# Kernel tuning notes

Hardware: AMD Instinct MI355X
Metric: run time of the kernel (lower is better)

The kernel has to match this reference:

```python
import jax, jax.numpy as jnp
import numpy as np

B, S, H = 2, 1024, 2048
D = 256          # index_dimension = min(index.embedding_dimension, hidden_size)
R = 32           # LoRA rank
K = 4            # index_k neighbors per query token
N_DB = 100000    # rows in the external index


def setup_inputs() -> dict:
    key = jax.random.key(0)
    ks = jax.random.split(key, 7)
    return {
        "hidden_states": jax.random.normal(ks[0], (B, S, H), jnp.float32),
        "db_keys": jax.random.normal(ks[1], (N_DB, D), jnp.float32),
        "db_values": jax.random.normal(ks[2], (N_DB, D), jnp.float32),
        "wq_in": jax.random.normal(ks[3], (H, R), jnp.float32) * 0.02,
        "wq_out": jax.random.normal(ks[4], (R, D), jnp.float32) * 0.02,
        "wv_in": jax.random.normal(ks[5], (D, R), jnp.float32) * 0.02,
        "wv_out": jax.random.normal(ks[6], (R, H), jnp.float32) * 0.02,
    }


def reference(hidden_states, db_keys, db_values, wq_in, wq_out, wv_in, wv_out):
    b, s, h = hidden_states.shape
    d = wq_out.shape[1]
    # query LoRA projection: hidden -> r -> index_dim
    q = (hidden_states @ wq_in) @ wq_out            # [B, S, D]

    # external k-NN lookup (exact L2 top-k over index table), no_grad in torch
    qf = q.reshape(b * s, d)                        # [B*S, D]
    qn = jnp.sum(qf * qf, axis=-1, keepdims=True)   # [B*S, 1]
    kn = jnp.sum(db_keys * db_keys, axis=-1)        # [N_DB]
    dist = qn - 2.0 * (qf @ db_keys.T) + kn[None, :]  # [B*S, N_DB]
    _, idx = jax.lax.top_k(-dist, K)                # [B*S, K] nearest neighbors

    # gather KV and reshape to [B, S*K, D] (matches torch view calls)
    kv_key = jax.lax.stop_gradient(db_keys[idx]).reshape(b, s * K, d)
    kv_val = jax.lax.stop_gradient(db_values[idx]).reshape(b, s * K, d)

    # SDPA, is_causal=True with Lq != Lk: top-left aligned tril mask (j <= i)
    scale = 1.0 / np.sqrt(d).astype(np.float32)
    scores = jnp.einsum('bqd,bkd->bqk', q, kv_key) * scale  # [B, S, S*K]
    mask = jnp.arange(s * K)[None, :] <= jnp.arange(s)[:, None]
    scores = jnp.where(mask[None, :, :], scores, jnp.finfo(scores.dtype).min)
    attn = jax.nn.softmax(scores, axis=-1)
    out = jnp.einsum('bqk,bkd->bqd', attn, kv_val)  # [B, S, D]

    # value LoRA projection: index_dim -> r -> hidden
    return (out @ wv_in) @ wv_out                   # [B, S, H]
```

## Files before the change

### kernel.cpp

```cpp
#include <hip/hip_runtime.h>
#include <cfloat>

#define B_   2
#define S_   1024
#define H_   2048
#define D_   256
#define R_   32
#define K_   4
#define NDB_ 100000

#define TSEL 256
#define NSEL (B_ * TSEL)

#define NCHUNK     112
#define CHUNK_ROWS 896
#define TILES      7
#define NT         128
#define MT         64
#define KC         64
#define LSTR       68

#define NEG_INF  (-3.0e38f)
#define IDX_MAX  0x7fffffff

#define TQ 4

#define OFF_Q     0
#define OFF_KN    0x200000
#define OFF_PS    0x280000
#define OFF_PI    0x360000
#define OFF_KVV   0x280000
#define OFF_KVT   0x480000
#define OFF_AO    0x680000
#define OFF_IDX   0x880000
#define OFF_CAND  0x890000
#define OFF_DBK16 0xA00000

typedef unsigned short ushort_t;
typedef unsigned int   uint_t;
typedef __attribute__((ext_vector_type(8)))  __bf16 bf16x8;
typedef __attribute__((ext_vector_type(16))) float  f32x16;

__device__ __forceinline__ void ins4(float sc, int n, float s[4], int id[4]) {
  if (sc > s[3] || (sc == s[3] && n < id[3])) {
    s[3] = sc; id[3] = n;
#pragma unroll
    for (int k = 3; k > 0; --k) {
      if (s[k] > s[k - 1] || (s[k] == s[k - 1] && id[k] < id[k - 1])) {
        float ts = s[k]; s[k] = s[k - 1]; s[k - 1] = ts;
        int ti = id[k]; id[k] = id[k - 1]; id[k - 1] = ti;
      }
    }
  }
}

__device__ __forceinline__ uint_t bfpack(float a, float b) {
  uint_t ua = __float_as_uint(a), ub = __float_as_uint(b);
  ua = (ua + 0x7fffu + ((ua >> 16) & 1u)) >> 16;
  ub = (ub + 0x7fffu + ((ub >> 16) & 1u)) >> 16;
  return ua | (ub << 16);
}

__global__ __launch_bounds__(256) void k_compute_q(
    const float* __restrict__ hidden, const float* __restrict__ wq_in,
    const float* __restrict__ wq_out, float* __restrict__ q) {
  __shared__ float hrow[H_];
  __shared__ float part[8][R_];
  __shared__ float q1[R_];
  const int m = blockIdx.x;
  const int t = threadIdx.x;
  const float* hp = hidden + (size_t)m * H_;
  ((float4*)hrow)[t]       = ((const float4*)hp)[t];
  ((float4*)hrow)[t + 256] = ((const float4*)hp)[t + 256];
  __syncthreads();
  const int r = t & 31, c = t >> 5;
  float p = 0.f;
#pragma unroll 4
  for (int e = c * 256; e < c * 256 + 256; ++e)
    p = fmaf(hrow[e], wq_in[(size_t)e * R_ + r], p);
  part[c][r] = p;
  __syncthreads();
  if (t < R_) {
    float s = 0.f;
#pragma unroll
    for (int cc = 0; cc < 8; ++cc) s += part[cc][t];
    q1[t] = s;
  }
  __syncthreads();
  float acc = 0.f;
#pragma unroll
  for (int rr = 0; rr < R_; ++rr) acc = fmaf(q1[rr], wq_out[rr * D_ + t], acc);
  q[(size_t)m * D_ + t] = acc;
}

__global__ __launch_bounds__(256) void k_kn_cvtT(const float* __restrict__ dbk,
                                                 float* __restrict__ kn,
                                                 ushort_t* __restrict__ dbk16T) {
  __shared__ float sT[32 * 256];
  const int n32 = blockIdx.x;
  const int t = threadIdx.x;
  {
    const int r = t >> 3, tc = t & 7;
    const float* rp = dbk + (size_t)(n32 * 32 + r) * D_;
    float s = 0.f;
#pragma unroll
    for (int k = 0; k < 8; ++k) {
      const int sl = tc + 8 * k;
      const float4 v = ((const float4*)rp)[sl];
      *(float4*)&sT[(r * 64 + (sl ^ (r & 7))) * 4] = v;
      s += v.x * v.x + v.y * v.y + v.z * v.z + v.w * v.w;
    }
    s += __shfl_down(s, 4, 8);
    s += __shfl_down(s, 2, 8);
    s += __shfl_down(s, 1, 8);
    if (tc == 0) kn[n32 * 32 + r] = s;
  }
  __syncthreads();
  {
    const int l = t & 63, w = t >> 6;
    const int row = l & 31, hc = l >> 5;
    uint4* dst = (uint4*)dbk16T + (size_t)n32 * 1024;
#pragma unroll
    for (int kk = 0; kk < 4; ++kk) {
      const int ks = kk * 4 + w;
      const int c = 2 * ks + hc;
      const int s0 = (2 * c) ^ (row & 7), s1 = (2 * c + 1) ^ (row & 7);
      const float4 a = *(const float4*)&sT[(row * 64 + s0) * 4];
      const float4 b = *(const float4*)&sT[(row * 64 + s1) * 4];
      uint4 pk;
      pk.x = bfpack(a.x, a.y); pk.y = bfpack(a.z, a.w);
      pk.z = bfpack(b.x, b.y); pk.w = bfpack(b.z, b.w);
      dst[(size_t)ks * 64 + l] = pk;
    }
  }
}

__global__ __launch_bounds__(256) void k_kn(const float* __restrict__ dbk,
                                            float* __restrict__ kn) {
  const int w = threadIdx.x >> 6, l = threadIdx.x & 63;
  const int n = blockIdx.x * 4 + w;
  if (n >= NDB_) return;
  const float4 v = ((const float4*)(dbk + (size_t)n * D_))[l];
  float s = v.x * v.x + v.y * v.y + v.z * v.z + v.w * v.w;
#pragma unroll
  for (int off = 32; off; off >>= 1) s += __shfl_down(s, off);
  if (l == 0) kn[n] = s;
}

__global__ __launch_bounds__(256, 4) void k_knn_mfma(
    const float* __restrict__ q, const ushort_t* __restrict__ dbk16T,
    const float* __restrict__ kn, float* __restrict__ pscore,
    int* __restrict__ pidx) {
  __shared__ __align__(16) char smem[32768 + CHUNK_ROWS * 4];
  ushort_t* sA  = (ushort_t*)smem;
  float*    knL = (float*)(smem + 32768);

  const int fid = blockIdx.x;
  const int xcd = fid & 7, idx8 = fid >> 3;
  const int chunk = xcd + 8 * (idx8 % 14);
  const int qb = idx8 / 14;

  const int tid = threadIdx.x;
  const int wv = tid >> 6, ln = tid & 63;
  const int lm = ln & 31, lh = ln >> 5;
  const int row_base = chunk * CHUNK_ROWS;

  {
    const int m = tid & 63, cg = tid >> 6;
    const int sq = qb * MT + m;
    const float* qp = q + ((size_t)((sq >> 8) * S_ + (sq & 255))) * D_;
#pragma unroll
    for (int cc = 0; cc < 8; ++cc) {
      const int c = cg * 8 + cc;
      const float4 v0 = *(const float4*)(qp + c * 8);
      const float4 v1 = *(const float4*)(qp + c * 8 + 4);
      uint4 pk;
      pk.x = bfpack(v0.x, v0.y); pk.y = bfpack(v0.z, v0.w);
      pk.z = bfpack(v1.x, v1.y); pk.w = bfpack(v1.z, v1.w);
      *(uint4*)&sA[(m * 32 + (c ^ (m & 7))) * 8] = pk;
    }
  }
  for (int j = tid; j < CHUNK_ROWS; j += 256) {
    int rr = row_base + j; if (rr >= NDB_) rr = NDB_ - 1;
    knL[j] = kn[rr];
  }
  __syncthreads();

  float s40[4], s41[4]; int i40[4], i41[4];
#pragma unroll
  for (int k = 0; k < 4; ++k) {
    s40[k] = NEG_INF; i40[k] = IDX_MAX;
    s41[k] = NEG_INF; i41[k] = IDX_MAX;
  }

  const int sw = lm & 7;
  const int abase0 = lm * 32;
  const int abase1 = (32 + lm) * 32;
  const int nbase = wv * 32 + 4 * lh;

  for (int tile = 0; tile < TILES; ++tile) {
    const int row0 = row_base + tile * NT;
    if (row0 >= NDB_) break;
    const int nw = row0 + wv * 32;
    if (nw >= NDB_) continue;

    f32x16 acc0, acc1;
#pragma unroll
    for (int r = 0; r < 16; ++r) { acc0[r] = 0.f; acc1[r] = 0.f; }

    const ushort_t* gw = dbk16T + (size_t)(nw >> 5) * 8192 + (size_t)ln * 8;
#pragma unroll
    for (int ks = 0; ks < 16; ++ks) {
      const bf16x8 bb = *(const bf16x8*)(gw + ks * 512);
      const int cs = (2 * ks + lh) ^ sw;
      const bf16x8 a0 = *(const bf16x8*)&sA[(abase0 + cs) * 8];
      const bf16x8 a1 = *(const bf16x8*)&sA[(abase1 + cs) * 8];
      acc0 = __builtin_amdgcn_mfma_f32_32x32x16_bf16(bb, a0, acc0, 0, 0, 0);
      acc1 = __builtin_amdgcn_mfma_f32_32x32x16_bf16(bb, a1, acc1, 0, 0, 0);
    }

#pragma unroll
    for (int g = 0; g < 4; ++g) {
      float v0[4], v1[4]; int nn[4];
#pragma unroll
      for (int j = 0; j < 4; ++j) {
        const int r = g * 4 + j;
        const int off = (r & 3) + 8 * (r >> 2);
        const int nloc = nbase + off;
        const float knv = knL[tile * 128 + nloc];
        const int n = row0 + nloc;
        nn[j] = n;
        const float x0 = fmaf(2.f, acc0[r], -knv);
        const float x1 = fmaf(2.f, acc1[r], -knv);
        const bool ok = n < NDB_;
        v0[j] = ok ? x0 : NEG_INF;
        v1[j] = ok ? x1 : NEG_INF;
      }
      const float m0 = fmaxf(fmaxf(v0[0], v0[1]), fmaxf(v0[2], v0[3]));
      if (m0 >= s40[3]) {
#pragma unroll
        for (int j = 0; j < 4; ++j) ins4(v0[j], nn[j], s40, i40);
      }
      const float m1 = fmaxf(fmaxf(v1[0], v1[1]), fmaxf(v1[2], v1[3]));
      if (m1 >= s41[3]) {
#pragma unroll
        for (int j = 0; j < 4; ++j) ins4(v1[j], nn[j], s41, i41);
      }
    }
  }

  __syncthreads();
  float* cs = (float*)smem;
  int*   ci = (int*)(smem + 8192);
  {
    const int st = wv * 2 + lh;
#pragma unroll
    for (int k = 0; k < 4; ++k) {
      cs[(lm * 8 + st) * 4 + k]        = s40[k];
      ci[(lm * 8 + st) * 4 + k]        = i40[k];
      cs[((32 + lm) * 8 + st) * 4 + k] = s41[k];
      ci[((32 + lm) * 8 + st) * 4 + k] = i41[k];
    }
  }
  __syncthreads();
  if (tid < 64) {
    float fs[4]; int fi[4];
#pragma unroll
    for (int k = 0; k < 4; ++k) { fs[k] = NEG_INF; fi[k] = IDX_MAX; }
    for (int c = 0; c < 32; ++c)
      ins4(cs[tid * 32 + c], ci[tid * 32 + c], fs, fi);
    const int sq = qb * MT + tid;
    float* po = pscore + ((size_t)sq * NCHUNK + chunk) * 4;
    int*   io = pidx   + ((size_t)sq * NCHUNK + chunk) * 4;
#pragma unroll
    for (int k = 0; k < 4; ++k) { po[k] = fs[k]; io[k] = fi[k]; }
  }
}

__global__ __launch_bounds__(256) void k_knn_partial(
    const float* __restrict__ q, const float* __restrict__ dbk,
    const float* __restrict__ kn, float* __restrict__ pscore,
    int* __restrict__ pidx) {
  __shared__ float smem[3 * KC * LSTR];
  float* sA  = smem;
  float* sB0 = smem + KC * LSTR;
  float* sB1 = smem + 2 * KC * LSTR;
  const int tid = threadIdx.x;
  const int tx = tid & 15, ty = tid >> 4;
  const int chunk = blockIdx.x, qb = blockIdx.y;
  const int arq = tid >> 2;
  const int aqd = (tid & 3) * 4;
  const int brk = tid >> 1;
  const int bh  = tid & 1;
  const int bcol = ((brk >> 3) << 2) | (brk & 3);
  float* sBw = (brk & 4) ? sB1 : sB0;
  const int sq_a = qb * MT + arq;
  const float* qsrc = q + ((size_t)((sq_a >> 8) * S_ + (sq_a & 255))) * D_;
  float s4[4][4]; int i4[4][4];
#pragma unroll
  for (int a = 0; a < 4; ++a)
#pragma unroll
    for (int b = 0; b < 4; ++b) { s4[a][b] = NEG_INF; i4[a][b] = IDX_MAX; }
  const int row_base = chunk * CHUNK_ROWS;
  for (int tile = 0; tile < TILES; ++tile) {
    const int row0 = row_base + tile * NT;
    if (row0 >= NDB_) break;
    int krow = row0 + brk; if (krow >= NDB_) krow = NDB_ - 1;
    const float* ksrc = dbk + (size_t)krow * D_;
    float acc[4][8];
#pragma unroll
    for (int a = 0; a < 4; ++a)
#pragma unroll
      for (int b = 0; b < 8; ++b) acc[a][b] = 0.f;
    for (int kc = 0; kc < 4; ++kc) {
      __syncthreads();
#pragma unroll
      for (int p = 0; p < 4; ++p) {
        const int kkl = p * 16 + aqd;
        const float4 v = *(const float4*)(qsrc + kc * KC + kkl);
        sA[(kkl + 0) * LSTR + arq] = v.x;
        sA[(kkl + 1) * LSTR + arq] = v.y;
        sA[(kkl + 2) * LSTR + arq] = v.z;
        sA[(kkl + 3) * LSTR + arq] = v.w;
      }
#pragma unroll
      for (int p = 0; p < 8; ++p) {
        const int kkl = bh * 32 + p * 4;
        const float4 v = *(const float4*)(ksrc + kc * KC + kkl);
        sBw[(kkl + 0) * LSTR + bcol] = v.x;
        sBw[(kkl + 1) * LSTR + bcol] = v.y;
        sBw[(kkl + 2) * LSTR + bcol] = v.z;
        sBw[(kkl + 3) * LSTR + bcol] = v.w;
      }
      __syncthreads();
#pragma unroll 4
      for (int kk = 0; kk < KC; ++kk) {
        const float4 a  = *(const float4*)&sA [kk * LSTR + ty * 4];
        const float4 b0 = *(const float4*)&sB0[kk * LSTR + tx * 4];
        const float4 b1 = *(const float4*)&sB1[kk * LSTR + tx * 4];
        const float av[4] = {a.x, a.y, a.z, a.w};
        const float bv[8] = {b0.x, b0.y, b0.z, b0.w, b1.x, b1.y, b1.z, b1.w};
#pragma unroll
        for (int qi = 0; qi < 4; ++qi)
#pragma unroll
          for (int nj = 0; nj < 8; ++nj)
            acc[qi][nj] = fmaf(av[qi], bv[nj], acc[qi][nj]);
      }
    }
#pragma unroll
    for (int nj = 0; nj < 8; ++nj) {
      const int n = row0 + tx * 8 + nj;
      if (n < NDB_) {
        const float knj = kn[n];
        ins4(2.f * acc[0][nj] - knj, n, s4[0], i4[0]);
        ins4(2.f * acc[1][nj] - knj, n, s4[1], i4[1]);
        ins4(2.f * acc[2][nj] - knj, n, s4[2], i4[2]);
        ins4(2.f * acc[3][nj] - knj, n, s4[3], i4[3]);
      }
    }
  }
  __syncthreads();
  float* cs = smem;
  int*   ci = (int*)(smem + 64 * 65);
#pragma unroll
  for (int qi = 0; qi < 4; ++qi)
#pragma unroll
    for (int k = 0; k < 4; ++k) {
      cs[(ty * 4 + qi) * 65 + tx * 4 + k] = s4[qi][k];
      ci[(ty * 4 + qi) * 65 + tx * 4 + k] = i4[qi][k];
    }
  __syncthreads();
  if (tid < 64) {
    float fs[4]; int fi[4];
#pragma unroll
    for (int k = 0; k < 4; ++k) { fs[k] = NEG_INF; fi[k] = IDX_MAX; }
    for (int c = 0; c < 64; ++c)
      ins4(cs[tid * 65 + c], ci[tid * 65 + c], fs, fi);
    const int sq = qb * MT + tid;
    float* po = pscore + ((size_t)sq * NCHUNK + chunk) * 4;
    int*   io = pidx   + ((size_t)sq * NCHUNK + chunk) * 4;
#pragma unroll
    for (int k = 0; k < 4; ++k) { po[k] = fs[k]; io[k] = fi[k]; }
  }
}

template <int RANKS>
__device__ __forceinline__ void merge_top(const float* __restrict__ pscore,
                                          const int* __restrict__ pidx,
                                          int* __restrict__ outp) {
  const int sq = blockIdx.x, l = threadIdx.x;
  float s4[4]; int i4[4];
#pragma unroll
  for (int k = 0; k < 4; ++k) { s4[k] = NEG_INF; i4[k] = IDX_MAX; }
  for (int c = l; c < NCHUNK * 4; c += 64)
    ins4(pscore[(size_t)sq * NCHUNK * 4 + c], pidx[(size_t)sq * NCHUNK * 4 + c], s4, i4);
#pragma unroll
  for (int r = 0; r < RANKS; ++r) {
    float s = s4[0]; int i = i4[0];
#pragma unroll
    for (int off = 32; off; off >>= 1) {
      float so = __shfl_down(s, off); int io = __shfl_down(i, off);
      if (so > s || (so == s && io < i)) { s = so; i = io; }
    }
    const float sw = __shfl(s, 0); const int iw = __shfl(i, 0);
    if (l == 0) outp[sq * RANKS + r] = iw;
    if (s4[0] == sw && i4[0] == iw) {
      s4[0] = s4[1]; i4[0] = i4[1];
      s4[1] = s4[2]; i4[1] = i4[2];
      s4[2] = s4[3]; i4[2] = i4[3];
      s4[3] = NEG_INF; i4[3] = IDX_MAX;
    }
  }
}

__global__ __launch_bounds__(64) void k_knn_merge4(const float* __restrict__ ps,
                                                   const int* __restrict__ pi,
                                                   int* __restrict__ knn_idx) {
  merge_top<4>(ps, pi, knn_idx);
}
__global__ __launch_bounds__(64) void k_knn_merge16(const float* __restrict__ ps,
                                                    const int* __restrict__ pi,
                                                    int* __restrict__ cand) {
  merge_top<16>(ps, pi, cand);
}

__global__ __launch_bounds__(256) void k_rescore(const float* __restrict__ q,
                                                 const float* __restrict__ dbk,
                                                 const float* __restrict__ kn,
                                                 const int* __restrict__ cand,
                                                 int* __restrict__ knn_idx) {
  __shared__ float scs[16];
  __shared__ int   sci[16];
  const int sq = blockIdx.x, wv = threadIdx.x >> 6, l = threadIdx.x & 63;
  const float* qp = q + ((size_t)((sq >> 8) * S_ + (sq & 255))) * D_;
  const float4 qv = ((const float4*)qp)[l];
  for (int cc = wv; cc < 16; cc += 4) {
    const int n = cand[sq * 16 + cc];
    const float4 kv = ((const float4*)(dbk + (size_t)n * D_))[l];
    float s = qv.x * kv.x + qv.y * kv.y + qv.z * kv.z + qv.w * kv.w;
#pragma unroll
    for (int off = 32; off; off >>= 1) s += __shfl_down(s, off);
    if (l == 0) { scs[cc] = 2.f * s - kn[n]; sci[cc] = n; }
  }
  __syncthreads();
  if (threadIdx.x == 0) {
    float s4[4]; int i4[4];
#pragma unroll
    for (int k = 0; k < 4; ++k) { s4[k] = NEG_INF; i4[k] = IDX_MAX; }
#pragma unroll
    for (int c = 0; c < 16; ++c) ins4(scs[c], sci[c], s4, i4);
#pragma unroll
    for (int k = 0; k < 4; ++k) knn_idx[sq * 4 + k] = i4[k];
  }
}

__global__ __launch_bounds__(256) void k_gather(const float* __restrict__ dbk,
                                                const float* __restrict__ dbv,
                                                const int* __restrict__ knn_idx,
                                                float* __restrict__ kvT,
                                                float* __restrict__ kvV) {
  const int b = blockIdx.x >> 6, j0 = (blockIdx.x & 63) * 16;
  const int w = threadIdx.x >> 6, l = threadIdx.x & 63;
  float* dstT = kvT + (size_t)b * D_ * 1024;
  float* dstV = kvV + (size_t)b * 1024 * D_;
  for (int jj = w; jj < 16; jj += 4) {
    const int j = j0 + jj;
    const int row = knn_idx[b * 1024 + j];
    const float4 kv = ((const float4*)(dbk + (size_t)row * D_))[l];
    dstT[(4 * l + 0) * 1024 + j] = kv.x;
    dstT[(4 * l + 1) * 1024 + j] = kv.y;
    dstT[(4 * l + 2) * 1024 + j] = kv.z;
    dstT[(4 * l + 3) * 1024 + j] = kv.w;
    const float4 vv = ((const float4*)(dbv + (size_t)row * D_))[l];
    ((float4*)(dstV + (size_t)j * D_))[l] = vv;
  }
}

template <int CMAX>
__device__ __forceinline__ void qk_dots(const float* __restrict__ kb, int t,
                                        const float (*qrow)[D_], float a[4][TQ]) {
#pragma unroll 2
  for (int d = 0; d < D_; d += 4) {
    float qv[TQ][4];
#pragma unroll
    for (int q = 0; q < TQ; ++q) {
      const float4 v = *(const float4*)&qrow[q][d];
      qv[q][0] = v.x; qv[q][1] = v.y; qv[q][2] = v.z; qv[q][3] = v.w;
    }
#pragma unroll
    for (int dd = 0; dd < 4; ++dd) {
      float kv[CMAX];
#pragma unroll
      for (int c = 0; c < CMAX; ++c)
        kv[c] = kb[(size_t)(d + dd) * 1024 + c * 256 + t];
#pragma unroll
      for (int c = 0; c < CMAX; ++c)
#pragma unroll
        for (int q = 0; q < TQ; ++q)
          a[c][q] = fmaf(qv[q][dd], kv[c], a[c][q]);
    }
  }
}

__global__ __launch_bounds__(256) void k_attn(const float* __restrict__ qarr,
                                              const float* __restrict__ kvT,
                                              const float* __restrict__ kvV,
                                              float* __restrict__ attout) {
  __shared__ float qrow[TQ][D_];
  __shared__ float attw[TQ][1024];
  __shared__ float pvred[4][TQ][D_];
  __shared__ float redm[4][TQ], reds[4][TQ];

  const int fid = blockIdx.x;
  const int b = fid & 1;
  const int g = fid >> 1;
  const int h = g >> 1;
  const int grp = (g & 1) ? (255 - h) : h;
  const int i0 = grp * TQ;
  const int t = threadIdx.x;
  const int w = t >> 6, l = t & 63;
  const int nkmax = i0 + TQ;
  const int cmax = (nkmax + 255) >> 8;

  {
    const float4 v = ((const float4*)(qarr + ((size_t)b * S_ + i0 + w) * D_))[l];
    float4 sv;
    sv.x = v.x * 0.0625f; sv.y = v.y * 0.0625f;
    sv.z = v.z * 0.0625f; sv.w = v.w * 0.0625f;
    ((float4*)&qrow[w][0])[l] = sv;
  }
  __syncthreads();

  const float* kb = kvT + (size_t)b * D_ * 1024;
  float a[4][TQ];
#pragma unroll
  for (int c = 0; c < 4; ++c)
#pragma unroll
    for (int q = 0; q < TQ; ++q) a[c][q] = 0.f;
  switch (cmax) {
    case 1: qk_dots<1>(kb, t, qrow, a); break;
    case 2: qk_dots<2>(kb, t, qrow, a); break;
    case 3: qk_dots<3>(kb, t, qrow, a); break;
    default: qk_dots<4>(kb, t, qrow, a); break;
  }
#pragma unroll
  for (int c = 0; c < 4; ++c)
    if (c < cmax)
#pragma unroll
      for (int q = 0; q < TQ; ++q)
        if (c * 256 + t > i0 + q) a[c][q] = NEG_INF;

  float M[TQ];
#pragma unroll
  for (int q = 0; q < TQ; ++q) {
    float m = NEG_INF;
    for (int c = 0; c < cmax; ++c) m = fmaxf(m, a[c][q]);
#pragma unroll
    for (int off = 32; off; off >>= 1) m = fmaxf(m, __shfl_down(m, off));
    if (l == 0) redm[w][q] = m;
  }
  __syncthreads();
#pragma unroll
  for (int q = 0; q < TQ; ++q)
    M[q] = fmaxf(fmaxf(redm[0][q], redm[1][q]), fmaxf(redm[2][q], redm[3][q]));
  float inv[TQ];
#pragma unroll
  for (int q = 0; q < TQ; ++q) {
    float s = 0.f;
    for (int c = 0; c < cmax; ++c) {
      const float p = (a[c][q] > 0.5f * NEG_INF) ? __expf(a[c][q] - M[q]) : 0.f;
      a[c][q] = p; s += p;
    }
#pragma unroll
    for (int off = 32; off; off >>= 1) s += __shfl_down(s, off);
    if (l == 0) reds[w][q] = s;
  }
  __syncthreads();
#pragma unroll
  for (int q = 0; q < TQ; ++q)
    inv[q] = 1.f / (reds[0][q] + reds[1][q] + reds[2][q] + reds[3][q]);
  for (int c = 0; c < cmax; ++c)
#pragma unroll
    for (int q = 0; q < TQ; ++q)
      attw[q][c * 256 + t] = a[c][q] * inv[q];
  __syncthreads();

  const float* vb = kvV + (size_t)b * 1024 * D_;
  float4 acc[TQ];
#pragma unroll
  for (int q = 0; q < TQ; ++q) acc[q] = make_float4(0.f, 0.f, 0.f, 0.f);
#pragma unroll 2
  for (int j = w; j < nkmax; j += 4) {
    const float4 v = ((const float4*)(vb + (size_t)j * D_))[l];
#pragma unroll
    for (int q = 0; q < TQ; ++q) {
      const float p = attw[q][j];
      acc[q].x = fmaf(p, v.x, acc[q].x);
      acc[q].y = fmaf(p, v.y, acc[q].y);
      acc[q].z = fmaf(p, v.z, acc[q].z);
      acc[q].w = fmaf(p, v.w, acc[q].w);
    }
  }
#pragma unroll
  for (int q = 0; q < TQ; ++q) ((float4*)&pvred[w][q][0])[l] = acc[q];
  __syncthreads();
  {
    const int q = t >> 6;
    float4 s = make_float4(0.f, 0.f, 0.f, 0.f);
#pragma unroll
    for (int ww = 0; ww < 4; ++ww) {
      const float4 p = ((const float4*)&pvred[ww][q][0])[l];
      s.x += p.x; s.y += p.y; s.z += p.z; s.w += p.w;
    }
    ((float4*)(attout + ((size_t)b * S_ + i0 + q) * D_))[l] = s;
  }
}

__global__ __launch_bounds__(256) void k_out(const float* __restrict__ attout,
                                             const float* __restrict__ wv_in,
                                             const float* __restrict__ wv_out,
                                             float* __restrict__ y) {
  __shared__ float row[D_];
  __shared__ float part[8][R_];
  __shared__ float t32[R_];
  const int m = blockIdx.x, t = threadIdx.x;
  row[t] = attout[(size_t)m * D_ + t];
  __syncthreads();
  const int r = t & 31, c = t >> 5;
  float p = 0.f;
#pragma unroll
  for (int d = c * 32; d < c * 32 + 32; ++d)
    p = fmaf(row[d], wv_in[d * R_ + r], p);
  part[c][r] = p;
  __syncthreads();
  if (t < R_) {
    float s = 0.f;
#pragma unroll
    for (int cc = 0; cc < 8; ++cc) s += part[cc][t];
    t32[t] = s;
  }
  __syncthreads();
  for (int hh = t; hh < H_; hh += 256) {
    float a = 0.f;
#pragma unroll
    for (int rr = 0; rr < R_; ++rr) a = fmaf(t32[rr], wv_out[rr * H_ + hh], a);
    y[(size_t)m * H_ + hh] = a;
  }
}

extern "C" void kernel_launch(void* const* d_in, const int* in_sizes, int n_in,
                              void* d_out, int out_size, void* d_ws, size_t ws_size,
                              hipStream_t stream) {
  const float* hidden  = (const float*)d_in[0];
  const float* db_keys = (const float*)d_in[1];
  const float* db_vals = (const float*)d_in[2];
  const float* wq_in   = (const float*)d_in[3];
  const float* wq_out  = (const float*)d_in[4];
  const float* wv_in   = (const float*)d_in[5];
  const float* wv_out  = (const float*)d_in[6];
  float* out = (float*)d_out;

  char* ws = (char*)d_ws;
  float*    q      = (float*)(ws + OFF_Q);
  float*    kn     = (float*)(ws + OFF_KN);
  float*    ps     = (float*)(ws + OFF_PS);
  int*      pi     = (int*)  (ws + OFF_PI);
  int*      idx    = (int*)  (ws + OFF_IDX);
  int*      cand   = (int*)  (ws + OFF_CAND);
  float*    kvT    = (float*)(ws + OFF_KVT);
  float*    attout = (float*)(ws + OFF_AO);
  float*    kvV    = (float*)(ws + OFF_KVV);
  ushort_t* dbk16  = (ushort_t*)(ws + OFF_DBK16);

  const size_t need = (size_t)OFF_DBK16 + (size_t)NDB_ * D_ * 2;

  k_compute_q<<<B_ * S_, 256, 0, stream>>>(hidden, wq_in, wq_out, q);
  if (ws_size >= need) {
    k_kn_cvtT<<<NDB_ / 32, 256, 0, stream>>>(db_keys, kn, dbk16);
    k_knn_mfma<<<NCHUNK * 8, 256, 0, stream>>>(q, dbk16, kn, ps, pi);
    k_knn_merge16<<<NSEL, 64, 0, stream>>>(ps, pi, cand);
    k_rescore<<<NSEL, 256, 0, stream>>>(q, db_keys, kn, cand, idx);
  } else {
    k_kn<<<(NDB_ + 3) / 4, 256, 0, stream>>>(db_keys, kn);
    k_knn_partial<<<dim3(NCHUNK, 8), 256, 0, stream>>>(q, db_keys, kn, ps, pi);
    k_knn_merge4<<<NSEL, 64, 0, stream>>>(ps, pi, idx);
  }
  k_gather<<<2 * 64, 256, 0, stream>>>(db_keys, db_vals, idx, kvT, kvV);
  k_attn<<<512, 256, 0, stream>>>(q, kvT, kvV, attout);
  k_out<<<B_ * S_, 256, 0, stream>>>(attout, wv_in, wv_out, out);
}
```

Baseline: 441.4 us.

## Fuse kNN merge, rescore and gather; fuse attention with output LoRA; prefetch keys

The kNN MFMA kernel now double-buffers its bf16 key fragments in registers, loading the next half-tile while the current one is multiplied. Its occupancy hint drops from 4 to 3 blocks to leave room for the extra registers. The merge16, rescore and gather kernels are combined into one finalize kernel that writes the gathered K/V directly. Attention is fused with the value LoRA projection, removing the attout buffer and the separate k_out launch. The aim is fewer launches, less intermediate global traffic, and hidden key-load latency, at the cost of higher register pressure and lower occupancy.

```diff
diff --git a/kernel.cpp b/kernel.cpp
--- a/kernel.cpp
+++ b/kernel.cpp
@@ -29,11 +29,9 @@
 #define OFF_KN    0x200000
 #define OFF_PS    0x280000
 #define OFF_PI    0x360000
-#define OFF_KVV   0x280000
 #define OFF_KVT   0x480000
-#define OFF_AO    0x680000
+#define OFF_KVV   0x680000
 #define OFF_IDX   0x880000
-#define OFF_CAND  0x890000
 #define OFF_DBK16 0xA00000
 
 typedef unsigned short ushort_t;
@@ -147,7 +145,7 @@
   if (l == 0) kn[n] = s;
 }
 
-__global__ __launch_bounds__(256, 4) void k_knn_mfma(
+__global__ __launch_bounds__(256, 3) void k_knn_mfma(
     const float* __restrict__ q, const ushort_t* __restrict__ dbk16T,
     const float* __restrict__ kn, float* __restrict__ pscore,
     int* __restrict__ pidx) {
@@ -197,26 +195,48 @@
   const int abase0 = lm * 32;
   const int abase1 = (32 + lm) * 32;
   const int nbase = wv * 32 + 4 * lh;
+  const int c32 = chunk * 28;
+
+#define LDF(buf, hs)                                                          \
+  {                                                                           \
+    int blk = c32 + ((hs) >> 1) * 4 + wv;                                     \
+    if (blk > NDB_ / 32 - 1) blk = NDB_ / 32 - 1;                             \
+    const ushort_t* gp =                                                      \
+        dbk16T + (size_t)blk * 8192 + ((hs) & 1) * 4096 + (size_t)ln * 8;     \
+    _Pragma("unroll") for (int i_ = 0; i_ < 8; ++i_)                          \
+        buf[i_] = *(const bf16x8*)(gp + i_ * 512);                            \
+  }
+
+  bf16x8 fA[8], fB[8];
+  LDF(fA, 0)
 
   for (int tile = 0; tile < TILES; ++tile) {
     const int row0 = row_base + tile * NT;
-    if (row0 >= NDB_) break;
-    const int nw = row0 + wv * 32;
-    if (nw >= NDB_) continue;
 
     f32x16 acc0, acc1;
 #pragma unroll
     for (int r = 0; r < 16; ++r) { acc0[r] = 0.f; acc1[r] = 0.f; }
 
-    const ushort_t* gw = dbk16T + (size_t)(nw >> 5) * 8192 + (size_t)ln * 8;
-#pragma unroll
-    for (int ks = 0; ks < 16; ++ks) {
-      const bf16x8 bb = *(const bf16x8*)(gw + ks * 512);
-      const int cs = (2 * ks + lh) ^ sw;
+    LDF(fB, 2 * tile + 1)
+#pragma unroll
+    for (int i = 0; i < 8; ++i) {
+      const int cs = (2 * i + lh) ^ sw;
       const bf16x8 a0 = *(const bf16x8*)&sA[(abase0 + cs) * 8];
       const bf16x8 a1 = *(const bf16x8*)&sA[(abase1 + cs) * 8];
-      acc0 = __builtin_amdgcn_mfma_f32_32x32x16_bf16(bb, a0, acc0, 0, 0, 0);
-      acc1 = __builtin_amdgcn_mfma_f32_32x32x16_bf16(bb, a1, acc1, 0, 0, 0);
+      acc0 = __builtin_amdgcn_mfma_f32_32x32x16_bf16(fA[i], a0, acc0, 0, 0, 0);
+      acc1 = __builtin_amdgcn_mfma_f32_32x32x16_bf16(fA[i], a1, acc1, 0, 0, 0);
+    }
+    {
+      const int hn = 2 * tile + 2;
+      LDF(fA, hn < 2 * TILES ? hn : 2 * TILES - 1)
+    }
+#pragma unroll
+    for (int i = 0; i < 8; ++i) {
+      const int cs = (2 * (8 + i) + lh) ^ sw;
+      const bf16x8 a0 = *(const bf16x8*)&sA[(abase0 + cs) * 8];
+      const bf16x8 a1 = *(const bf16x8*)&sA[(abase1 + cs) * 8];
+      acc0 = __builtin_amdgcn_mfma_f32_32x32x16_bf16(fB[i], a0, acc0, 0, 0, 0);
+      acc1 = __builtin_amdgcn_mfma_f32_32x32x16_bf16(fB[i], a1, acc1, 0, 0, 0);
     }
 
 #pragma unroll
@@ -248,6 +268,7 @@
       }
     }
   }
+#undef LDF
 
   __syncthreads();
   float* cs = (float*)smem;
@@ -384,10 +405,9 @@
   }
 }
 
-template <int RANKS>
-__device__ __forceinline__ void merge_top(const float* __restrict__ pscore,
-                                          const int* __restrict__ pidx,
-                                          int* __restrict__ outp) {
+__global__ __launch_bounds__(64) void k_knn_merge4(const float* __restrict__ pscore,
+                                                   const int* __restrict__ pidx,
+                                                   int* __restrict__ knn_idx) {
   const int sq = blockIdx.x, l = threadIdx.x;
   float s4[4]; int i4[4];
 #pragma unroll
@@ -395,7 +415,7 @@
   for (int c = l; c < NCHUNK * 4; c += 64)
     ins4(pscore[(size_t)sq * NCHUNK * 4 + c], pidx[(size_t)sq * NCHUNK * 4 + c], s4, i4);
 #pragma unroll
-  for (int r = 0; r < RANKS; ++r) {
+  for (int r = 0; r < 4; ++r) {
     float s = s4[0]; int i = i4[0];
 #pragma unroll
     for (int off = 32; off; off >>= 1) {
@@ -403,7 +423,7 @@
       if (so > s || (so == s && io < i)) { s = so; i = io; }
     }
     const float sw = __shfl(s, 0); const int iw = __shfl(i, 0);
-    if (l == 0) outp[sq * RANKS + r] = iw;
+    if (l == 0) knn_idx[sq * 4 + r] = iw;
     if (s4[0] == sw && i4[0] == iw) {
       s4[0] = s4[1]; i4[0] = i4[1];
       s4[1] = s4[2]; i4[1] = i4[2];
@@ -413,29 +433,49 @@
   }
 }
 
-__global__ __launch_bounds__(64) void k_knn_merge4(const float* __restrict__ ps,
-                                                   const int* __restrict__ pi,
-                                                   int* __restrict__ knn_idx) {
-  merge_top<4>(ps, pi, knn_idx);
-}
-__global__ __launch_bounds__(64) void k_knn_merge16(const float* __restrict__ ps,
-                                                    const int* __restrict__ pi,
-                                                    int* __restrict__ cand) {
-  merge_top<16>(ps, pi, cand);
-}
-
-__global__ __launch_bounds__(256) void k_rescore(const float* __restrict__ q,
-                                                 const float* __restrict__ dbk,
-                                                 const float* __restrict__ kn,
-                                                 const int* __restrict__ cand,
-                                                 int* __restrict__ knn_idx) {
+__global__ __launch_bounds__(256) void k_finalize(
+    const float* __restrict__ pscore, const int* __restrict__ pidx,
+    const float* __restrict__ q, const float* __restrict__ dbk,
+    const float* __restrict__ dbv, const float* __restrict__ kn,
+    float* __restrict__ kvT, float* __restrict__ kvV) {
+  __shared__ int   cand16[16];
   __shared__ float scs[16];
   __shared__ int   sci[16];
-  const int sq = blockIdx.x, wv = threadIdx.x >> 6, l = threadIdx.x & 63;
+  __shared__ int   top4[4];
+  const int sq = blockIdx.x;
+  const int t = threadIdx.x, wv = t >> 6, l = t & 63;
+
+  if (wv == 0) {
+    float s4[4]; int i4[4];
+#pragma unroll
+    for (int k = 0; k < 4; ++k) { s4[k] = NEG_INF; i4[k] = IDX_MAX; }
+    for (int c = l; c < NCHUNK * 4; c += 64)
+      ins4(pscore[(size_t)sq * NCHUNK * 4 + c],
+           pidx[(size_t)sq * NCHUNK * 4 + c], s4, i4);
+#pragma unroll
+    for (int r = 0; r < 16; ++r) {
+      float s = s4[0]; int i = i4[0];
+#pragma unroll
+      for (int off = 32; off; off >>= 1) {
+        float so = __shfl_down(s, off); int io = __shfl_down(i, off);
+        if (so > s || (so == s && io < i)) { s = so; i = io; }
+      }
+      const float sw = __shfl(s, 0); const int iw = __shfl(i, 0);
+      if (l == 0) cand16[r] = iw;
+      if (s4[0] == sw && i4[0] == iw) {
+        s4[0] = s4[1]; i4[0] = i4[1];
+        s4[1] = s4[2]; i4[1] = i4[2];
+        s4[2] = s4[3]; i4[2] = i4[3];
+        s4[3] = NEG_INF; i4[3] = IDX_MAX;
+      }
+    }
+  }
+  __syncthreads();
+
   const float* qp = q + ((size_t)((sq >> 8) * S_ + (sq & 255))) * D_;
   const float4 qv = ((const float4*)qp)[l];
   for (int cc = wv; cc < 16; cc += 4) {
-    const int n = cand[sq * 16 + cc];
+    const int n = cand16[cc];
     const float4 kv = ((const float4*)(dbk + (size_t)n * D_))[l];
     float s = qv.x * kv.x + qv.y * kv.y + qv.z * kv.z + qv.w * kv.w;
 #pragma unroll
@@ -443,15 +483,28 @@
     if (l == 0) { scs[cc] = 2.f * s - kn[n]; sci[cc] = n; }
   }
   __syncthreads();
-  if (threadIdx.x == 0) {
+  if (t == 0) {
     float s4[4]; int i4[4];
 #pragma unroll
     for (int k = 0; k < 4; ++k) { s4[k] = NEG_INF; i4[k] = IDX_MAX; }
 #pragma unroll
     for (int c = 0; c < 16; ++c) ins4(scs[c], sci[c], s4, i4);
 #pragma unroll
-    for (int k = 0; k < 4; ++k) knn_idx[sq * 4 + k] = i4[k];
-  }
+    for (int k = 0; k < 4; ++k) top4[k] = i4[k];
+  }
+  __syncthreads();
+
+  const int b = sq >> 8, tok = sq & 255;
+  const int j = tok * 4 + wv;
+  const int row = top4[wv];
+  float* dstT = kvT + (size_t)b * D_ * 1024;
+  const float4 kvk = ((const float4*)(dbk + (size_t)row * D_))[l];
+  dstT[(4 * l + 0) * 1024 + j] = kvk.x;
+  dstT[(4 * l + 1) * 1024 + j] = kvk.y;
+  dstT[(4 * l + 2) * 1024 + j] = kvk.z;
+  dstT[(4 * l + 3) * 1024 + j] = kvk.w;
+  const float4 vv = ((const float4*)(dbv + (size_t)row * D_))[l];
+  ((float4*)(kvV + ((size_t)b * 1024 + j) * D_))[l] = vv;
 }
 
 __global__ __launch_bounds__(256) void k_gather(const float* __restrict__ dbk,
@@ -502,14 +555,15 @@
   }
 }
 
-__global__ __launch_bounds__(256) void k_attn(const float* __restrict__ qarr,
-                                              const float* __restrict__ kvT,
-                                              const float* __restrict__ kvV,
-                                              float* __restrict__ attout) {
+__global__ __launch_bounds__(256) void k_attn_out(
+    const float* __restrict__ qarr, const float* __restrict__ kvT,
+    const float* __restrict__ kvV, const float* __restrict__ wv_in,
+    const float* __restrict__ wv_out, float* __restrict__ y) {
   __shared__ float qrow[TQ][D_];
   __shared__ float attw[TQ][1024];
   __shared__ float pvred[4][TQ][D_];
   __shared__ float redm[4][TQ], reds[4][TQ];
+  __shared__ float t32s[TQ][R_];
 
   const int fid = blockIdx.x;
   const int b = fid & 1;
@@ -550,7 +604,6 @@
       for (int q = 0; q < TQ; ++q)
         if (c * 256 + t > i0 + q) a[c][q] = NEG_INF;
 
-  float M[TQ];
 #pragma unroll
   for (int q = 0; q < TQ; ++q) {
     float m = NEG_INF;
@@ -560,6 +613,7 @@
     if (l == 0) redm[w][q] = m;
   }
   __syncthreads();
+  float M[TQ];
 #pragma unroll
   for (int q = 0; q < TQ; ++q)
     M[q] = fmaxf(fmaxf(redm[0][q], redm[1][q]), fmaxf(redm[2][q], redm[3][q]));
@@ -605,46 +659,44 @@
   for (int q = 0; q < TQ; ++q) ((float4*)&pvred[w][q][0])[l] = acc[q];
   __syncthreads();
   {
-    const int q = t >> 6;
+    const int qq = t >> 6;
     float4 s = make_float4(0.f, 0.f, 0.f, 0.f);
 #pragma unroll
     for (int ww = 0; ww < 4; ++ww) {
-      const float4 p = ((const float4*)&pvred[ww][q][0])[l];
+      const float4 p = ((const float4*)&pvred[ww][qq][0])[l];
       s.x += p.x; s.y += p.y; s.z += p.z; s.w += p.w;
     }
-    ((float4*)(attout + ((size_t)b * S_ + i0 + q) * D_))[l] = s;
-  }
-}
-
-__global__ __launch_bounds__(256) void k_out(const float* __restrict__ attout,
-                                             const float* __restrict__ wv_in,
-                                             const float* __restrict__ wv_out,
-                                             float* __restrict__ y) {
-  __shared__ float row[D_];
-  __shared__ float part[8][R_];
-  __shared__ float t32[R_];
-  const int m = blockIdx.x, t = threadIdx.x;
-  row[t] = attout[(size_t)m * D_ + t];
-  __syncthreads();
-  const int r = t & 31, c = t >> 5;
-  float p = 0.f;
-#pragma unroll
-  for (int d = c * 32; d < c * 32 + 32; ++d)
-    p = fmaf(row[d], wv_in[d * R_ + r], p);
-  part[c][r] = p;
-  __syncthreads();
-  if (t < R_) {
-    float s = 0.f;
-#pragma unroll
-    for (int cc = 0; cc < 8; ++cc) s += part[cc][t];
-    t32[t] = s;
-  }
-  __syncthreads();
-  for (int hh = t; hh < H_; hh += 256) {
-    float a = 0.f;
-#pragma unroll
-    for (int rr = 0; rr < R_; ++rr) a = fmaf(t32[rr], wv_out[rr * H_ + hh], a);
-    y[(size_t)m * H_ + hh] = a;
+    ((float4*)&qrow[qq][0])[l] = s;
+  }
+  __syncthreads();
+
+  {
+    const int qq = t >> 6, r = l & 31, hh = l >> 5;
+    float p = 0.f;
+    const float* ar = &qrow[qq][hh * 128];
+    const float* wp = wv_in + (size_t)(hh * 128) * R_ + r;
+#pragma unroll 8
+    for (int d = 0; d < 128; ++d) p = fmaf(ar[d], wp[(size_t)d * R_], p);
+    p += __shfl_down(p, 32);
+    if (l < 32) t32s[qq][r] = p;
+  }
+  __syncthreads();
+
+  const size_t ybase = ((size_t)b * S_ + i0) * H_;
+  for (int ho = t; ho < H_; ho += 256) {
+    float a0 = 0.f, a1 = 0.f, a2 = 0.f, a3 = 0.f;
+#pragma unroll
+    for (int rr = 0; rr < R_; ++rr) {
+      const float wvv = wv_out[rr * H_ + ho];
+      a0 = fmaf(t32s[0][rr], wvv, a0);
+      a1 = fmaf(t32s[1][rr], wvv, a1);
+      a2 = fmaf(t32s[2][rr], wvv, a2);
+      a3 = fmaf(t32s[3][rr], wvv, a3);
+    }
+    y[ybase + ho]           = a0;
+    y[ybase + H_ + ho]      = a1;
+    y[ybase + 2 * H_ + ho]  = a2;
+    y[ybase + 3 * H_ + ho]  = a3;
   }
 }
 
@@ -666,9 +718,7 @@
   float*    ps     = (float*)(ws + OFF_PS);
   int*      pi     = (int*)  (ws + OFF_PI);
   int*      idx    = (int*)  (ws + OFF_IDX);
-  int*      cand   = (int*)  (ws + OFF_CAND);
   float*    kvT    = (float*)(ws + OFF_KVT);
-  float*    attout = (float*)(ws + OFF_AO);
   float*    kvV    = (float*)(ws + OFF_KVV);
   ushort_t* dbk16  = (ushort_t*)(ws + OFF_DBK16);
 
@@ -678,14 +728,12 @@
   if (ws_size >= need) {
     k_kn_cvtT<<<NDB_ / 32, 256, 0, stream>>>(db_keys, kn, dbk16);
     k_knn_mfma<<<NCHUNK * 8, 256, 0, stream>>>(q, dbk16, kn, ps, pi);
-    k_knn_merge16<<<NSEL, 64, 0, stream>>>(ps, pi, cand);
-    k_rescore<<<NSEL, 256, 0, stream>>>(q, db_keys, kn, cand, idx);
+    k_finalize<<<NSEL, 256, 0, stream>>>(ps, pi, q, db_keys, db_vals, kn, kvT, kvV);
   } else {
     k_kn<<<(NDB_ + 3) / 4, 256, 0, stream>>>(db_keys, kn);
     k_knn_partial<<<dim3(NCHUNK, 8), 256, 0, stream>>>(q, db_keys, kn, ps, pi);
     k_knn_merge4<<<NSEL, 64, 0, stream>>>(ps, pi, idx);
-  }
-  k_gather<<<2 * 64, 256, 0, stream>>>(db_keys, db_vals, idx, kvT, kvV);
-  k_attn<<<512, 256, 0, stream>>>(q, kvT, kvV, attout);
-  k_out<<<B_ * S_, 256, 0, stream>>>(attout, wv_in, wv_out, out);
-}
+    k_gather<<<2 * 64, 256, 0, stream>>>(db_keys, db_vals, idx, kvT, kvV);
+  }
+  k_attn_out<<<512, 256, 0, stream>>>(q, kvT, kvV, wv_in, wv_out, out);
+}
```

Result: slower. 562.0 us (+27.3%).
